# Performance work log

Measured on AMD Instinct MI355X. Metric: run time of the kernel, lower is better.

Reference implementation:

```python
import jax, jax.numpy as jnp
import numpy as np

SIZE = 224
SCALE = (0.1, 1.0)
RATIO = (0.8, 1.25)
N_TRIES = 10


def _get_params(key, H, W):
    """Batched RandomResizedCrop params. H, W: int32 [B]. Returns int32 (i, j, h, w)."""
    B = H.shape[0]
    Hf = H.astype(jnp.float32)
    Wf = W.astype(jnp.float32)
    area = Hf * Wf
    log_lo = np.log(RATIO[0]).astype(np.float32)
    log_hi = np.log(RATIO[1]).astype(np.float32)
    final_h = jnp.full((B,), -1.0, dtype=jnp.float32)
    final_w = jnp.full((B,), -1.0, dtype=jnp.float32)
    final_i = jnp.full((B,), -1.0, dtype=jnp.float32)
    final_j = jnp.full((B,), -1.0, dtype=jnp.float32)
    success = jnp.zeros((B,), dtype=bool)
    for t in range(N_TRIES):  # fixed small trip count, matches torch loop
        k1, k2, k3, k4 = jax.random.split(jax.random.fold_in(key, t), 4)
        target_area = area * jax.random.uniform(k1, (B,), minval=SCALE[0], maxval=SCALE[1])
        aspect = jnp.exp(jax.random.uniform(k2, (B,), minval=log_lo, maxval=log_hi))
        crop_w = jnp.round(jnp.sqrt(target_area * aspect))
        crop_h = jnp.round(jnp.sqrt(target_area / aspect))
        valid = (crop_w > 0) & (crop_w <= Wf) & (crop_h > 0) & (crop_h <= Hf) & (~success)
        max_i = jnp.clip(Hf - crop_h + 1.0, 1.0, None)
        max_j = jnp.clip(Wf - crop_w + 1.0, 1.0, None)
        rand_i = jnp.floor(jax.random.uniform(k3, (B,)) * max_i)
        rand_j = jnp.floor(jax.random.uniform(k4, (B,)) * max_j)
        final_h = jnp.where(valid, crop_h, final_h)
        final_w = jnp.where(valid, crop_w, final_w)
        final_i = jnp.where(valid, rand_i, final_i)
        final_j = jnp.where(valid, rand_j, final_j)
        success = success | valid
    # center-crop fallback for failed samples
    failed = ~success
    in_ratio = Wf / Hf
    fb_w = jnp.where(in_ratio > RATIO[1], jnp.round(Hf * RATIO[1]), Wf)
    fb_h = jnp.where(in_ratio < RATIO[0], jnp.round(Wf / RATIO[0]), Hf)
    fb_i = jnp.floor((Hf - fb_h) / 2.0)
    fb_j = jnp.floor((Wf - fb_w) / 2.0)
    final_h = jnp.where(failed, fb_h, final_h)
    final_w = jnp.where(failed, fb_w, final_w)
    final_i = jnp.where(failed, fb_i, final_i)
    final_j = jnp.where(failed, fb_j, final_j)
    return (final_i.astype(jnp.int32), final_j.astype(jnp.int32),
            final_h.astype(jnp.int32), final_w.astype(jnp.int32))


def _bilinear_crop_resize(img, i, j, h, w):
    """Crop img[C,Hm,Wm] at (i,j,h,w) then bilinear-resize to (SIZE,SIZE).
    Matches torch F.interpolate(bilinear, align_corners=False) coordinate mapping."""
    C, Hm, Wm = img.shape
    hf = h.astype(jnp.float32)
    wf = w.astype(jnp.float32)
    # source coords within the crop, clamped as torch does
    ys = jnp.clip((jnp.arange(SIZE, dtype=jnp.float32) + 0.5) * hf / SIZE - 0.5, 0.0, hf - 1.0)
    xs = jnp.clip((jnp.arange(SIZE, dtype=jnp.float32) + 0.5) * wf / SIZE - 0.5, 0.0, wf - 1.0)
    y0f = jnp.floor(ys); x0f = jnp.floor(xs)
    wy = ys - y0f; wx = xs - x0f
    y0 = jnp.clip(y0f.astype(jnp.int32) + i, 0, Hm - 1)
    y1 = jnp.clip(y0 + 1, 0, jnp.clip(i + h - 1, 0, Hm - 1))
    x0 = jnp.clip(x0f.astype(jnp.int32) + j, 0, Wm - 1)
    x1 = jnp.clip(x0 + 1, 0, jnp.clip(j + w - 1, 0, Wm - 1))
    g00 = img[:, y0[:, None], x0[None, :]]  # [C,SIZE,SIZE]
    g01 = img[:, y0[:, None], x1[None, :]]
    g10 = img[:, y1[:, None], x0[None, :]]
    g11 = img[:, y1[:, None], x1[None, :]]
    top = (1.0 - wx)[None, None, :] * g00 + wx[None, None, :] * g01
    bot = (1.0 - wx)[None, None, :] * g10 + wx[None, None, :] * g11
    return (1.0 - wy)[None, :, None] * top + wy[None, :, None] * bot


def setup_inputs() -> dict:
    B, C, Hm, Wm_meta = 64, 3, 512, 513
    key = jax.random.key(0)
    k1, k2, k3 = jax.random.split(key, 3)
    x = jax.random.normal(k1, (B, C, Hm, Wm_meta), dtype=jnp.float32)
    H_orig = jax.random.randint(k2, (B,), 256, Hm + 1).astype(jnp.float32)
    W_orig = jax.random.randint(k3, (B,), 256, (Wm_meta - 1) + 1).astype(jnp.float32)
    # metadata column: per-sample original dims
    x = x.at[:, 0, 0, -1].set(H_orig)
    x = x.at[:, 1, 0, -1].set(W_orig)
    return {"x": x}


def reference(x):
    B, C, Hm, Wm_meta = x.shape
    Wm = Wm_meta - 1
    # decode original dims from metadata (before flip, as in torch code)
    H = x[:, 0, 0, -1].astype(jnp.int32)
    W = x[:, 1, 0, -1].astype(jnp.int32)
    key = jax.random.key(42)
    kflip, kparams = jax.random.split(key)
    flip_mask = jax.random.uniform(kflip, (B,)) > 0.5
    # hflip the full tensor (including meta column), faithful to original
    x = jnp.where(flip_mask[:, None, None, None], x[:, :, :, ::-1], x)
    i, j, h, w = _get_params(kparams, H, W)
    x_no_meta = x[:, :, :, :Wm]
    return jax.vmap(_bilinear_crop_resize)(x_no_meta, i, j, h, w)
```

## Files before the change

kernel.cpp:

```cpp
#include <hip/hip_runtime.h>
#include <stdint.h>

#define B_DIM 64
#define C_DIM 3
#define HM 512
#define WM_META 513
#define WM 512
#define OSIZE 224
#define N_TRIES 10

__device__ __forceinline__ uint32_t rotl32(uint32_t v, int d) {
    return (v << d) | (v >> (32 - d));
}

__device__ __forceinline__ void threefry2x32(uint32_t k0, uint32_t k1,
                                             uint32_t x0, uint32_t x1,
                                             uint32_t& o0, uint32_t& o1) {
    const uint32_t ks0 = k0, ks1 = k1, ks2 = k0 ^ k1 ^ 0x1BD11BDAu;
    x0 += ks0; x1 += ks1;
    x0 += x1; x1 = rotl32(x1, 13); x1 ^= x0;
    x0 += x1; x1 = rotl32(x1, 15); x1 ^= x0;
    x0 += x1; x1 = rotl32(x1, 26); x1 ^= x0;
    x0 += x1; x1 = rotl32(x1,  6); x1 ^= x0;
    x0 += ks1; x1 += ks2 + 1u;
    x0 += x1; x1 = rotl32(x1, 17); x1 ^= x0;
    x0 += x1; x1 = rotl32(x1, 29); x1 ^= x0;
    x0 += x1; x1 = rotl32(x1, 16); x1 ^= x0;
    x0 += x1; x1 = rotl32(x1, 24); x1 ^= x0;
    x0 += ks2; x1 += ks0 + 2u;
    x0 += x1; x1 = rotl32(x1, 13); x1 ^= x0;
    x0 += x1; x1 = rotl32(x1, 15); x1 ^= x0;
    x0 += x1; x1 = rotl32(x1, 26); x1 ^= x0;
    x0 += x1; x1 = rotl32(x1,  6); x1 ^= x0;
    x0 += ks0; x1 += ks1 + 3u;
    x0 += x1; x1 = rotl32(x1, 17); x1 ^= x0;
    x0 += x1; x1 = rotl32(x1, 29); x1 ^= x0;
    x0 += x1; x1 = rotl32(x1, 16); x1 ^= x0;
    x0 += x1; x1 = rotl32(x1, 24); x1 ^= x0;
    x0 += ks1; x1 += ks2 + 4u;
    x0 += x1; x1 = rotl32(x1, 13); x1 ^= x0;
    x0 += x1; x1 = rotl32(x1, 15); x1 ^= x0;
    x0 += x1; x1 = rotl32(x1, 26); x1 ^= x0;
    x0 += x1; x1 = rotl32(x1,  6); x1 ^= x0;
    x0 += ks2; x1 += ks0 + 5u;
    o0 = x0; o1 = x1;
}

__device__ __forceinline__ float jax_uniform_elem(uint32_t k0, uint32_t k1, int b,
                                                  float lo, float hi) {
#pragma clang fp contract(off)
    uint32_t w0, w1;
    threefry2x32(k0, k1, 0u, (uint32_t)b, w0, w1);
    uint32_t bits = w0 ^ w1;
    uint32_t fb = (bits >> 9) | 0x3f800000u;
    float u = __uint_as_float(fb) - 1.0f;
    float d = hi - lo;
    float v = u * d + lo;
    return fmaxf(lo, v);
}

__global__ void __launch_bounds__(64)
params_kernel(const float* __restrict__ x, int* __restrict__ params) {
#pragma clang fp contract(off)
    int b = threadIdx.x;
    if (b >= B_DIM) return;

    uint32_t kf0, kf1, kp0, kp1;
    threefry2x32(0u, 42u, 0u, 0u, kf0, kf1);
    threefry2x32(0u, 42u, 0u, 1u, kp0, kp1);

    float uf = jax_uniform_elem(kf0, kf1, b, 0.0f, 1.0f);
    int flip = (uf > 0.5f) ? 1 : 0;

    size_t base = (size_t)b * C_DIM * HM * WM_META;
    float Hf = x[base + (WM_META - 1)];
    float Wf = x[base + (size_t)HM * WM_META + (WM_META - 1)];
    float area = Hf * Wf;

    const float log_lo = -0.22314355131420976f;
    const float log_hi =  0.22314355131420976f;

    float fi = -1.0f, fj = -1.0f, fh = -1.0f, fw = -1.0f;
    bool success = false;

    for (int t = 0; t < N_TRIES; ++t) {
        uint32_t f0, f1;
        threefry2x32(kp0, kp1, 0u, (uint32_t)t, f0, f1);
        uint32_t k10, k11, k20, k21, k30, k31, k40, k41;
        threefry2x32(f0, f1, 0u, 0u, k10, k11);
        threefry2x32(f0, f1, 0u, 1u, k20, k21);
        threefry2x32(f0, f1, 0u, 2u, k30, k31);
        threefry2x32(f0, f1, 0u, 3u, k40, k41);

        float u1 = jax_uniform_elem(k10, k11, b, 0.1f, 1.0f);
        float u2 = jax_uniform_elem(k20, k21, b, log_lo, log_hi);
        float u3 = jax_uniform_elem(k30, k31, b, 0.0f, 1.0f);
        float u4 = jax_uniform_elem(k40, k41, b, 0.0f, 1.0f);

        float ta = area * u1;
        float aspect = expf(u2);
        float cw = rintf(sqrtf(ta * aspect));
        float ch = rintf(sqrtf(ta / aspect));

        bool valid = (cw > 0.0f) && (cw <= Wf) && (ch > 0.0f) && (ch <= Hf) && (!success);

        float max_i = fmaxf(Hf - ch + 1.0f, 1.0f);
        float max_j = fmaxf(Wf - cw + 1.0f, 1.0f);
        float ri = floorf(u3 * max_i);
        float rj = floorf(u4 * max_j);

        if (valid) { fh = ch; fw = cw; fi = ri; fj = rj; success = true; }
    }

    if (!success) {
        float in_ratio = Wf / Hf;
        float fbw = (in_ratio > 1.25f) ? rintf(Hf * 1.25f) : Wf;
        float fbh = (in_ratio < 0.8f)  ? rintf(Wf / 0.8f)  : Hf;
        fi = floorf((Hf - fbh) / 2.0f);
        fj = floorf((Wf - fbw) / 2.0f);
        fh = fbh; fw = fbw;
    }

    params[b * 5 + 0] = flip;
    params[b * 5 + 1] = (int)fi;
    params[b * 5 + 2] = (int)fj;
    params[b * 5 + 3] = (int)fh;
    params[b * 5 + 4] = (int)fw;
}

__global__ void __launch_bounds__(256)
resize_kernel(const float* __restrict__ x, const int* __restrict__ params,
              float* __restrict__ out) {
#pragma clang fp contract(off)
    const int OX_UNITS = OSIZE / 4;
    int idx = blockIdx.x * 256 + threadIdx.x;
    const int total = B_DIM * C_DIM * OSIZE * OX_UNITS;
    if (idx >= total) return;

    int oxu = idx % OX_UNITS;
    int tmp = idx / OX_UNITS;
    int oy = tmp % OSIZE;
    tmp /= OSIZE;
    int c = tmp % C_DIM;
    int b = tmp / C_DIM;

    int flip = params[b * 5 + 0];
    int pi   = params[b * 5 + 1];
    int pj   = params[b * 5 + 2];
    int ph   = params[b * 5 + 3];
    int pw   = params[b * 5 + 4];

    float hf = (float)ph, wf = (float)pw;

    float ys = ((float)oy + 0.5f) * hf;
    ys = ys / 224.0f;
    ys = ys - 0.5f;
    ys = fminf(fmaxf(ys, 0.0f), hf - 1.0f);
    float y0f = floorf(ys);
    float wy = ys - y0f;
    int y0 = (int)y0f + pi;
    y0 = min(max(y0, 0), HM - 1);
    int yhi = min(max(pi + ph - 1, 0), HM - 1);
    int y1 = min(max(y0 + 1, 0), yhi);

    int xhi = min(max(pj + pw - 1, 0), WM - 1);

    const float* img  = x + ((size_t)(b * C_DIM + c)) * HM * WM_META;
    const float* row0 = img + (size_t)y0 * WM_META;
    const float* row1 = img + (size_t)y1 * WM_META;

    float res[4];
#pragma unroll
    for (int k = 0; k < 4; ++k) {
        int ox = oxu * 4 + k;
        float xs = ((float)ox + 0.5f) * wf;
        xs = xs / 224.0f;
        xs = xs - 0.5f;
        xs = fminf(fmaxf(xs, 0.0f), wf - 1.0f);
        float x0f = floorf(xs);
        float wx = xs - x0f;
        int x0 = (int)x0f + pj;
        x0 = min(max(x0, 0), WM - 1);
        int x1 = min(max(x0 + 1, 0), xhi);

        int mx0 = flip ? (WM - x0) : x0;
        int mx1 = flip ? (WM - x1) : x1;

        float g00 = row0[mx0];
        float g01 = row0[mx1];
        float g10 = row1[mx0];
        float g11 = row1[mx1];

        float top = (1.0f - wx) * g00 + wx * g01;
        float bot = (1.0f - wx) * g10 + wx * g11;
        res[k] = (1.0f - wy) * top + wy * bot;
    }

    float4 v = make_float4(res[0], res[1], res[2], res[3]);
    *reinterpret_cast<float4*>(out + (size_t)idx * 4) = v;
}

extern "C" void kernel_launch(void* const* d_in, const int* in_sizes, int n_in,
                              void* d_out, int out_size, void* d_ws, size_t ws_size,
                              hipStream_t stream) {
    const float* x = (const float*)d_in[0];
    float* out = (float*)d_out;
    int* params = (int*)d_ws;

    params_kernel<<<1, 64, 0, stream>>>(x, params);

    const int total = B_DIM * C_DIM * OSIZE * (OSIZE / 4);
    const int blocks = (total + 255) / 256;
    resize_kernel<<<blocks, 256, 0, stream>>>(x, params, out);
}
```

Measured before the change: 276.6 us.

## Fuse crop-parameter generation into resize kernel, parallelizing RNG across threads

```diff
diff --git a/kernel.cpp b/kernel.cpp
--- a/kernel.cpp
+++ b/kernel.cpp
@@ -8,6 +8,9 @@
 #define WM 512
 #define OSIZE 224
 #define N_TRIES 10
+#define OX_UNITS (OSIZE / 4)
+#define UNITS_PER_B (C_DIM * OSIZE * OX_UNITS)
+#define BLOCKS_PER_B (UNITS_PER_B / 256)
 
 __device__ __forceinline__ uint32_t rotl32(uint32_t v, int d) {
     return (v << d) | (v >> (32 - d));
@@ -46,12 +49,14 @@
     o0 = x0; o1 = x1;
 }
 
-__device__ __forceinline__ float jax_uniform_elem(uint32_t k0, uint32_t k1, int b,
-                                                  float lo, float hi) {
-#pragma clang fp contract(off)
+__device__ __forceinline__ uint32_t jax_bits_elem(uint32_t k0, uint32_t k1, int b) {
     uint32_t w0, w1;
     threefry2x32(k0, k1, 0u, (uint32_t)b, w0, w1);
-    uint32_t bits = w0 ^ w1;
+    return w0 ^ w1;
+}
+
+__device__ __forceinline__ float bits_to_uniform(uint32_t bits, float lo, float hi) {
+#pragma clang fp contract(off)
     uint32_t fb = (bits >> 9) | 0x3f800000u;
     float u = __uint_as_float(fb) - 1.0f;
     float d = hi - lo;
@@ -59,43 +64,53 @@
     return fmaxf(lo, v);
 }
 
-__global__ void __launch_bounds__(64)
-params_kernel(const float* __restrict__ x, int* __restrict__ params) {
+__global__ void __launch_bounds__(256)
+fused_kernel(const float* __restrict__ x, float* __restrict__ out) {
 #pragma clang fp contract(off)
-    int b = threadIdx.x;
-    if (b >= B_DIM) return;
-
-    uint32_t kf0, kf1, kp0, kp1;
-    threefry2x32(0u, 42u, 0u, 0u, kf0, kf1);
-    threefry2x32(0u, 42u, 0u, 1u, kp0, kp1);
-
-    float uf = jax_uniform_elem(kf0, kf1, b, 0.0f, 1.0f);
-    int flip = (uf > 0.5f) ? 1 : 0;
+    __shared__ float u_lds[41];
+
+    const int tid = threadIdx.x;
+    const int b = blockIdx.x / BLOCKS_PER_B;
+
+    if (tid < 41) {
+        if (tid < 40) {
+            int t = tid >> 2;
+            int q = tid & 3;
+            uint32_t kp0, kp1;
+            threefry2x32(0u, 42u, 0u, 1u, kp0, kp1);
+            uint32_t f0, f1;
+            threefry2x32(kp0, kp1, 0u, (uint32_t)t, f0, f1);
+            uint32_t kq0, kq1;
+            threefry2x32(f0, f1, 0u, (uint32_t)q, kq0, kq1);
+            uint32_t bits = jax_bits_elem(kq0, kq1, b);
+            const float log_lo = -0.22314355131420976f;
+            const float log_hi =  0.22314355131420976f;
+            float lo = (q == 0) ? 0.1f : (q == 1) ? log_lo : 0.0f;
+            float hi = (q == 0) ? 1.0f : (q == 1) ? log_hi : 1.0f;
+            u_lds[tid] = bits_to_uniform(bits, lo, hi);
+        } else {
+            uint32_t kf0, kf1;
+            threefry2x32(0u, 42u, 0u, 0u, kf0, kf1);
+            uint32_t bits = jax_bits_elem(kf0, kf1, b);
+            u_lds[40] = bits_to_uniform(bits, 0.0f, 1.0f);
+        }
+    }
+    __syncthreads();
 
     size_t base = (size_t)b * C_DIM * HM * WM_META;
     float Hf = x[base + (WM_META - 1)];
     float Wf = x[base + (size_t)HM * WM_META + (WM_META - 1)];
     float area = Hf * Wf;
 
-    const float log_lo = -0.22314355131420976f;
-    const float log_hi =  0.22314355131420976f;
+    int flip = (u_lds[40] > 0.5f) ? 1 : 0;
 
     float fi = -1.0f, fj = -1.0f, fh = -1.0f, fw = -1.0f;
     bool success = false;
-
     for (int t = 0; t < N_TRIES; ++t) {
-        uint32_t f0, f1;
-        threefry2x32(kp0, kp1, 0u, (uint32_t)t, f0, f1);
-        uint32_t k10, k11, k20, k21, k30, k31, k40, k41;
-        threefry2x32(f0, f1, 0u, 0u, k10, k11);
-        threefry2x32(f0, f1, 0u, 1u, k20, k21);
-        threefry2x32(f0, f1, 0u, 2u, k30, k31);
-        threefry2x32(f0, f1, 0u, 3u, k40, k41);
-
-        float u1 = jax_uniform_elem(k10, k11, b, 0.1f, 1.0f);
-        float u2 = jax_uniform_elem(k20, k21, b, log_lo, log_hi);
-        float u3 = jax_uniform_elem(k30, k31, b, 0.0f, 1.0f);
-        float u4 = jax_uniform_elem(k40, k41, b, 0.0f, 1.0f);
+        float u1 = u_lds[t * 4 + 0];
+        float u2 = u_lds[t * 4 + 1];
+        float u3 = u_lds[t * 4 + 2];
+        float u4 = u_lds[t * 4 + 3];
 
         float ta = area * u1;
         float aspect = expf(u2);
@@ -111,7 +126,6 @@
 
         if (valid) { fh = ch; fw = cw; fi = ri; fj = rj; success = true; }
     }
-
     if (!success) {
         float in_ratio = Wf / Hf;
         float fbw = (in_ratio > 1.25f) ? rintf(Hf * 1.25f) : Wf;
@@ -121,34 +135,14 @@
         fh = fbh; fw = fbw;
     }
 
-    params[b * 5 + 0] = flip;
-    params[b * 5 + 1] = (int)fi;
-    params[b * 5 + 2] = (int)fj;
-    params[b * 5 + 3] = (int)fh;
-    params[b * 5 + 4] = (int)fw;
-}
-
-__global__ void __launch_bounds__(256)
-resize_kernel(const float* __restrict__ x, const int* __restrict__ params,
-              float* __restrict__ out) {
-#pragma clang fp contract(off)
-    const int OX_UNITS = OSIZE / 4;
-    int idx = blockIdx.x * 256 + threadIdx.x;
-    const int total = B_DIM * C_DIM * OSIZE * OX_UNITS;
-    if (idx >= total) return;
-
+    int pi = (int)fi, pj = (int)fj, ph = (int)fh, pw = (int)fw;
+
+    int idx = blockIdx.x * 256 + tid;
     int oxu = idx % OX_UNITS;
     int tmp = idx / OX_UNITS;
     int oy = tmp % OSIZE;
     tmp /= OSIZE;
     int c = tmp % C_DIM;
-    int b = tmp / C_DIM;
-
-    int flip = params[b * 5 + 0];
-    int pi   = params[b * 5 + 1];
-    int pj   = params[b * 5 + 2];
-    int ph   = params[b * 5 + 3];
-    int pw   = params[b * 5 + 4];
 
     float hf = (float)ph, wf = (float)pw;
 
@@ -205,11 +199,7 @@
                               hipStream_t stream) {
     const float* x = (const float*)d_in[0];
     float* out = (float*)d_out;
-    int* params = (int*)d_ws;
-
-    params_kernel<<<1, 64, 0, stream>>>(x, params);
-
-    const int total = B_DIM * C_DIM * OSIZE * (OSIZE / 4);
-    const int blocks = (total + 255) / 256;
-    resize_kernel<<<blocks, 256, 0, stream>>>(x, params, out);
-}
+
+    const int blocks = B_DIM * BLOCKS_PER_B;
+    fused_kernel<<<blocks, 256, 0, stream>>>(x, out);
+}
```

Result: no change. 275.3 us (-0.5%).
